# Performance work log

Measured on AMD Instinct MI355X. Metric: run time of the kernel, lower is better.

Reference implementation:

```python
import jax, jax.numpy as jnp
import numpy as np

K_TOP = 8
TEMP = 1.0
GUMBEL_EPS = 1e-20
GEN_EPS = 1e-7
NEG_INF = -1e9


def _genconv(xn, src, dst, e, We, be, W1, b1, W2, b2):
    """GENConv: edge-proj, m=relu(x_src+e)+eps, per-dst softmax aggregation (t=1),
    residual add, then 2-layer MLP."""
    N = xn.shape[0]
    ep = e @ We + be                         # [E, C]
    m = jax.nn.relu(xn[src] + ep) + GEN_EPS  # [E, C]
    mx = jax.ops.segment_max(m, dst, num_segments=N)
    mx = jnp.where(jnp.isfinite(mx), mx, 0.0)
    w = jnp.exp(m - mx[dst])
    den = jax.ops.segment_sum(w, dst, num_segments=N)
    agg = jax.ops.segment_sum(w * m, dst, num_segments=N) / jnp.where(den > 0, den, 1.0)
    out = agg + xn
    return jax.nn.relu(out @ W1 + b1) @ W2 + b2


def setup_inputs() -> dict:
    key = jax.random.key(0)
    ks = jax.random.split(key, 16)
    N, E, D, ED = 1024, 16384, 128, 16
    H1, H2, OUT = 64, 64, 40
    s = 0.02
    return {
        "x": jax.random.normal(ks[0], (N, D), jnp.float32),
        "edge_attr": jax.random.normal(ks[1], (E, ED), jnp.float32),
        "gumbel_u": jax.random.uniform(ks[2], (N, N), jnp.float32),
        "mlp_w": jax.random.normal(ks[3], (ED + 2 * D, 1), jnp.float32) * s,
        "mlp_b": jnp.zeros((1,), jnp.float32),
        "c1_we": jax.random.normal(ks[4], (ED, D), jnp.float32) * s,
        "c1_be": jnp.zeros((D,), jnp.float32),
        "c1_w1": jax.random.normal(ks[5], (D, 2 * D), jnp.float32) * s,
        "c1_b1": jnp.zeros((2 * D,), jnp.float32),
        "c1_w2": jax.random.normal(ks[6], (2 * D, H1), jnp.float32) * s,
        "c1_b2": jnp.zeros((H1,), jnp.float32),
        "c2_we": jax.random.normal(ks[7], (ED, H1), jnp.float32) * s,
        "c2_be": jnp.zeros((H1,), jnp.float32),
        "c2_w1": jax.random.normal(ks[8], (H1, 2 * H1), jnp.float32) * s,
        "c2_b1": jnp.zeros((2 * H1,), jnp.float32),
        "c2_w2": jax.random.normal(ks[9], (2 * H1, H2), jnp.float32) * s,
        "c2_b2": jnp.zeros((H2,), jnp.float32),
        "fc_w": jax.random.normal(ks[10], (H2, OUT), jnp.float32) * s,
        "fc_b": jnp.zeros((OUT,), jnp.float32),
        "num_nodes": N,
        "edge_index": jax.random.randint(ks[11], (2, E), 0, N),
        "node_mask": jnp.ones((N,), jnp.int32),
    }


def reference(x, edge_attr, gumbel_u, mlp_w, mlp_b,
              c1_we, c1_be, c1_w1, c1_b1, c1_w2, c1_b2,
              c2_we, c2_be, c2_w1, c2_b1, c2_w2, c2_b2,
              fc_w, fc_b, num_nodes, edge_index, node_mask):
    N, D = x.shape
    src, dst = edge_index[0], edge_index[1]

    # dense adjacency (duplicate edges sum, only used as a zero/nonzero mask)
    adj = jnp.zeros((N, N), x.dtype).at[src, dst].add(1.0)

    # Edge-score MLP on concat([x_u, x_v*mask, edge_attr_dense]) decomposed
    # linearly (same math as scoring the dense [N,N,2D+ED] feature tensor).
    w_node, w_nb, w_e = mlp_w[:D], mlp_w[D:2 * D], mlp_w[2 * D:]
    s_edge = jnp.zeros((N, N), x.dtype).at[src, dst].set((edge_attr @ w_e)[:, 0])
    score = (x @ w_node) + (x @ w_nb).T * (adj > 0) + s_edge + mlp_b[0]
    score = jnp.where(adj == 0, NEG_INF, score)

    z = jax.nn.softmax(score, axis=-1)
    g = -jnp.log(-jnp.log(gumbel_u + GUMBEL_EPS) + GUMBEL_EPS)
    z = jax.nn.softmax((z + g) / TEMP, axis=-1)

    # top-k edge sampling; softmax output is strictly positive so valid_mask
    # (z>0) is always all-True and shapes stay static at N*k edges.
    _, topi = jax.lax.top_k(z, K_TOP)                       # [N, k]
    new_src = jnp.repeat(jnp.arange(N), K_TOP)
    new_dst = topi.reshape(-1)

    # match each new edge against old edge list (argmax of boolean equality,
    # unmatched edges fall back to index 0 exactly as torch argmax does)
    eq = (edge_index[0][None, :] == new_src[:, None]) & \
         (edge_index[1][None, :] == new_dst[:, None])       # [N*k, E]
    new_attr = edge_attr[jnp.argmax(eq, axis=-1)]

    h = _genconv(x, new_src, new_dst, new_attr, c1_we, c1_be, c1_w1, c1_b1, c1_w2, c1_b2)
    h = jax.nn.relu(h)
    h = _genconv(h, new_src, new_dst, new_attr, c2_we, c2_be, c2_w1, c2_b1, c2_w2, c2_b2)
    h = jax.nn.relu(h)
    out = h @ fc_w + fc_b
    # node_mask is all ones, so x[node_mask != 0] == identity; masked write
    # keeps static shapes under jit.
    return jnp.where((node_mask != 0)[:, None], out, 0.0)
```

## Files before the change

### kernel.cpp

```cpp
#include <hip/hip_runtime.h>
#include <cfloat>

#define NN   1024
#define NE   16384
#define D0   128
#define EDIM 16
#define NH1  64
#define NOUT 40
#define KTOP 8
#define NEGINF (-1000000000.0f)
#define MAXDEG 64
#define PMAX   64

#define OFF_EM  0u
#define OFF_ND  32768u
#define OFF_H   65536u

__device__ __forceinline__ void amx(float& v, int& j, float ov, int oj) {
    if (ov > v || (ov == v && oj < j)) { v = ov; j = oj; }
}

__global__ __launch_bounds__(512) void topk_kernel(
    const float* __restrict__ x, const float* __restrict__ ea,
    const float* __restrict__ u, const float* __restrict__ mlp_w,
    const float* __restrict__ mlp_b, const int* __restrict__ ei,
    const float* __restrict__ c1w1,
    int* __restrict__ nd, int* __restrict__ em)
{
    __shared__ int   idmx[NN];
    __shared__ int   idmn[NN];
    __shared__ float sv[NN];
    __shared__ int   plj[PMAX];
    __shared__ int   ple[PMAX];
    __shared__ int   np;
    __shared__ float wred[16];
    __shared__ float candv[64];
    __shared__ int   candj[64];
    const int i = blockIdx.x, t = threadIdx.x;
    const int lane = t & 63, w = t >> 6;
    const int subl = t & 15;
    const int gg = t >> 4;

    float uval[2];
    uval[0] = u[i * NN + w * 128 + lane];
    uval[1] = u[i * NN + w * 128 + 64 + lane];

    #pragma unroll
    for (int q = 0; q < 2; q++) {
        int j = t + q * 512;
        idmx[j] = -1; idmn[j] = 0x7FFFFFFF; sv[j] = NEGINF;
    }
    if (t == 0) np = 0;
    __syncthreads();

    const int4* s4 = (const int4*)ei;
    #pragma unroll
    for (int q = 0; q < 8; q++) {
        int idx4 = t + q * 512;
        int4 sv4 = s4[idx4];
        int e0 = idx4 * 4;
        if (sv4.x == i) { int dj = ei[NE + e0 + 0]; atomicMax(&idmx[dj], e0 + 0); atomicMin(&idmn[dj], e0 + 0); }
        if (sv4.y == i) { int dj = ei[NE + e0 + 1]; atomicMax(&idmx[dj], e0 + 1); atomicMin(&idmn[dj], e0 + 1); }
        if (sv4.z == i) { int dj = ei[NE + e0 + 2]; atomicMax(&idmx[dj], e0 + 2); atomicMin(&idmn[dj], e0 + 2); }
        if (sv4.w == i) { int dj = ei[NE + e0 + 3]; atomicMax(&idmx[dj], e0 + 3); atomicMin(&idmn[dj], e0 + 3); }
    }
    __syncthreads();

    #pragma unroll
    for (int q = 0; q < 2; q++) {
        int j = t + q * 512;
        int e = idmx[j];
        if (e >= 0) {
            int p = atomicAdd(&np, 1);
            if (p < PMAX) { plj[p] = j; ple[p] = e; }
        }
    }
    __syncthreads();

    float part = x[i * D0 + lane] * mlp_w[lane] + x[i * D0 + 64 + lane] * mlp_w[64 + lane];
    for (int s2 = 32; s2; s2 >>= 1) part += __shfl_down(part, s2);
    const float arb = __shfl(part, 0) + mlp_b[0];

    const int npc = min(np, PMAX);
    for (int p = gg; p < npc; p += 32) {
        int j = plj[p], e = ple[p];
        float pp = ea[e * EDIM + subl] * mlp_w[2 * D0 + subl];
        #pragma unroll
        for (int k = 0; k < 8; k++)
            pp += x[j * D0 + subl + k * 16] * mlp_w[D0 + subl + k * 16];
        #pragma unroll
        for (int s2 = 8; s2; s2 >>= 1) pp += __shfl_down(pp, s2, 16);
        if (subl == 0) sv[j] = pp + arb;
    }
    __syncthreads();

    float val[2];
    val[0] = sv[w * 128 + lane];
    val[1] = sv[w * 128 + 64 + lane];
    float lm = fmaxf(val[0], val[1]);
    for (int s2 = 32; s2; s2 >>= 1) lm = fmaxf(lm, __shfl_down(lm, s2));
    if (lane == 0) wred[w] = lm;
    __syncthreads();
    float rowmax = wred[0];
    #pragma unroll
    for (int q = 1; q < 8; q++) rowmax = fmaxf(rowmax, wred[q]);
    const bool noedge = (rowmax == NEGINF);

    float ls = 0.f;
    #pragma unroll
    for (int q = 0; q < 2; q++) {
        float ev = noedge ? 1.0f : ((val[q] == NEGINF) ? 0.0f : expf(val[q] - rowmax));
        val[q] = ev; ls += ev;
    }
    for (int s2 = 32; s2; s2 >>= 1) ls += __shfl_down(ls, s2);
    if (lane == 0) wred[8 + w] = ls;
    __syncthreads();
    float rsum = wred[8];
    #pragma unroll
    for (int q = 1; q < 8; q++) rsum += wred[8 + q];

    #pragma unroll
    for (int q = 0; q < 2; q++) {
        float g = -logf(-logf(uval[q] + 1e-20f) + 1e-20f);
        val[q] = val[q] / rsum + g;
    }

    for (int sel = 0; sel < KTOP; sel++) {
        float bv = -FLT_MAX; int bj = NN;
        amx(bv, bj, val[0], w * 128 + lane);
        amx(bv, bj, val[1], w * 128 + 64 + lane);
        for (int s2 = 32; s2; s2 >>= 1) {
            float ov = __shfl_down(bv, s2); int oj = __shfl_down(bj, s2);
            amx(bv, bj, ov, oj);
        }
        int wj = __shfl(bj, 0);
        if (lane == 0) { candv[w * KTOP + sel] = bv; candj[w * KTOP + sel] = bj; }
        if (w * 128 + lane == wj) val[0] = -FLT_MAX;
        if (w * 128 + 64 + lane == wj) val[1] = -FLT_MAX;
    }
    __syncthreads();

    if (w == 0) {
        float mv = candv[lane];
        int   mj = candj[lane];
        for (int sel = 0; sel < KTOP; sel++) {
            float bv = mv; int bj = mj;
            for (int s2 = 32; s2; s2 >>= 1) {
                float ov = __shfl_down(bv, s2); int oj = __shfl_down(bj, s2);
                amx(bv, bj, ov, oj);
            }
            int wj = __shfl(bj, 0);
            if (lane == 0) {
                int mn = idmn[wj];
                em[i * KTOP + sel] = (mn == 0x7FFFFFFF) ? 0 : mn;
                nd[i * KTOP + sel] = wj;
            }
            if (mj == wj) mv = -FLT_MAX;
        }
    } else {
        float pf = 0.f;
        if (t < 192)       pf = x[i * D0 + (t - 64)];
        else if (t < 448)  pf = ea[i * 256 + (t - 192)];
        else if (t < 480)  pf = c1w1[i * 32 + (t - 448)];
        asm volatile("" :: "v"(pf));
    }
}

__global__ __launch_bounds__(256) void genconv1_kernel(
    const float* __restrict__ x, const float* __restrict__ ea,
    const float* __restrict__ we_g, const float* __restrict__ be,
    const float* __restrict__ w1, const float* __restrict__ b1,
    const float* __restrict__ w2, const float* __restrict__ b2,
    const int* __restrict__ nd, const int* __restrict__ em,
    float* __restrict__ h)
{
    __shared__ int   slots[MAXDEG];
    __shared__ float eatt[MAXDEG * EDIM];
    __shared__ float arow[D0];
    __shared__ float t1s[2 * D0];
    __shared__ int   cnt_s;
    const int t = threadIdx.x;
    const int r = blockIdx.x;
    if (t == 0) cnt_s = 0;
    __syncthreads();

    const int4* nd4 = (const int4*)nd;
    #pragma unroll
    for (int q = 0; q < 8; q++) {
        int idx4 = t + q * 256;
        int4 v = nd4[idx4];
        int n0 = idx4 * 4;
        if (v.x == r) { int p = atomicAdd(&cnt_s, 1); if (p < MAXDEG) slots[p] = n0 + 0; }
        if (v.y == r) { int p = atomicAdd(&cnt_s, 1); if (p < MAXDEG) slots[p] = n0 + 1; }
        if (v.z == r) { int p = atomicAdd(&cnt_s, 1); if (p < MAXDEG) slots[p] = n0 + 2; }
        if (v.w == r) { int p = atomicAdd(&cnt_s, 1); if (p < MAXDEG) slots[p] = n0 + 3; }
    }
    __syncthreads();
    const int cnt = min(cnt_s, MAXDEG);
    if (t == 0) {
        for (int p = 1; p < cnt; p++) {
            int v = slots[p]; int q = p - 1;
            while (q >= 0 && slots[q] > v) { slots[q + 1] = slots[q]; q--; }
            slots[q + 1] = v;
        }
    }
    __syncthreads();
    for (int q = t; q < cnt * EDIM; q += 256)
        eatt[q] = ea[em[slots[q >> 4]] * EDIM + (q & 15)];
    __syncthreads();

    if (t < D0) {
        const int d = t;
        float wed[EDIM];
        #pragma unroll
        for (int k = 0; k < EDIM; k++) wed[k] = we_g[k * D0 + d];
        const float bed = be[d];

        float mxv = -FLT_MAX;
        for (int idx = 0; idx < cnt; idx++) {
            int src = slots[idx] >> 3;
            float ep = bed;
            #pragma unroll
            for (int k = 0; k < EDIM; k++) ep += eatt[idx * EDIM + k] * wed[k];
            float m = fmaxf(x[src * D0 + d] + ep, 0.f) + 1e-7f;
            mxv = fmaxf(mxv, m);
        }
        float den = 0.f, num = 0.f;
        for (int idx = 0; idx < cnt; idx++) {
            int src = slots[idx] >> 3;
            float ep = bed;
            #pragma unroll
            for (int k = 0; k < EDIM; k++) ep += eatt[idx * EDIM + k] * wed[k];
            float m = fmaxf(x[src * D0 + d] + ep, 0.f) + 1e-7f;
            float w = expf(m - mxv);
            den += w; num += w * m;
        }
        float agg = cnt ? num / (den > 0.f ? den : 1.f) : 0.f;
        arow[d] = agg + x[r * D0 + d];
    }
    __syncthreads();

    {
        float acc = b1[t];
        for (int k = 0; k < D0; k++) acc += arow[k] * w1[k * 2 * D0 + t];
        t1s[t] = fmaxf(acc, 0.f);
    }
    __syncthreads();
    if (t < NH1) {
        float acc = b2[t];
        for (int k = 0; k < 2 * D0; k++) acc += t1s[k] * w2[k * NH1 + t];
        h[r * NH1 + t] = fmaxf(acc, 0.f);
    }
}

__global__ __launch_bounds__(256) void genconv2_kernel(
    const float* __restrict__ h, const float* __restrict__ ea,
    const float* __restrict__ we_g, const float* __restrict__ be,
    const float* __restrict__ w1, const float* __restrict__ b1,
    const float* __restrict__ w2, const float* __restrict__ b2,
    const float* __restrict__ fcw, const float* __restrict__ fcb,
    const int* __restrict__ nd, const int* __restrict__ em,
    const int* __restrict__ mask, float* __restrict__ out)
{
    __shared__ int   slots[MAXDEG];
    __shared__ float eatt[MAXDEG * EDIM];
    __shared__ float arow[NH1];
    __shared__ float t2s[2 * NH1];
    __shared__ float h2s[NH1];
    __shared__ int   cnt_s;
    const int t = threadIdx.x;
    const int r = blockIdx.x;
    if (t == 0) cnt_s = 0;
    __syncthreads();

    const int4* nd4 = (const int4*)nd;
    #pragma unroll
    for (int q = 0; q < 8; q++) {
        int idx4 = t + q * 256;
        int4 v = nd4[idx4];
        int n0 = idx4 * 4;
        if (v.x == r) { int p = atomicAdd(&cnt_s, 1); if (p < MAXDEG) slots[p] = n0 + 0; }
        if (v.y == r) { int p = atomicAdd(&cnt_s, 1); if (p < MAXDEG) slots[p] = n0 + 1; }
        if (v.z == r) { int p = atomicAdd(&cnt_s, 1); if (p < MAXDEG) slots[p] = n0 + 2; }
        if (v.w == r) { int p = atomicAdd(&cnt_s, 1); if (p < MAXDEG) slots[p] = n0 + 3; }
    }
    __syncthreads();
    const int cnt = min(cnt_s, MAXDEG);
    if (t == 0) {
        for (int p = 1; p < cnt; p++) {
            int v = slots[p]; int q = p - 1;
            while (q >= 0 && slots[q] > v) { slots[q + 1] = slots[q]; q--; }
            slots[q + 1] = v;
        }
    }
    __syncthreads();
    for (int q = t; q < cnt * EDIM; q += 256)
        eatt[q] = ea[em[slots[q >> 4]] * EDIM + (q & 15)];
    __syncthreads();

    if (t < NH1) {
        const int d = t;
        float wed[EDIM];
        #pragma unroll
        for (int k = 0; k < EDIM; k++) wed[k] = we_g[k * NH1 + d];
        const float bed = be[d];

        float mxv = -FLT_MAX;
        for (int idx = 0; idx < cnt; idx++) {
            int src = slots[idx] >> 3;
            float ep = bed;
            #pragma unroll
            for (int k = 0; k < EDIM; k++) ep += eatt[idx * EDIM + k] * wed[k];
            float m = fmaxf(h[src * NH1 + d] + ep, 0.f) + 1e-7f;
            mxv = fmaxf(mxv, m);
        }
        float den = 0.f, num = 0.f;
        for (int idx = 0; idx < cnt; idx++) {
            int src = slots[idx] >> 3;
            float ep = bed;
            #pragma unroll
            for (int k = 0; k < EDIM; k++) ep += eatt[idx * EDIM + k] * wed[k];
            float m = fmaxf(h[src * NH1 + d] + ep, 0.f) + 1e-7f;
            float w = expf(m - mxv);
            den += w; num += w * m;
        }
        float agg = cnt ? num / (den > 0.f ? den : 1.f) : 0.f;
        arow[d] = agg + h[r * NH1 + d];
    }
    __syncthreads();

    if (t < 2 * NH1) {
        float acc = b1[t];
        for (int k = 0; k < NH1; k++) acc += arow[k] * w1[k * 2 * NH1 + t];
        t2s[t] = fmaxf(acc, 0.f);
    }
    __syncthreads();
    if (t < NH1) {
        float acc = b2[t];
        for (int k = 0; k < 2 * NH1; k++) acc += t2s[k] * w2[k * NH1 + t];
        h2s[t] = fmaxf(acc, 0.f);
    }
    __syncthreads();
    if (t < NOUT) {
        float acc = fcb[t];
        for (int k = 0; k < NH1; k++) acc += h2s[k] * fcw[k * NOUT + t];
        out[r * NOUT + t] = (mask[r] != 0) ? acc : 0.f;
    }
}

extern "C" void kernel_launch(void* const* d_in, const int* in_sizes, int n_in,
                              void* d_out, int out_size, void* d_ws, size_t ws_size,
                              hipStream_t stream) {
    const float* x      = (const float*)d_in[0];
    const float* ea     = (const float*)d_in[1];
    const float* u      = (const float*)d_in[2];
    const float* mlp_w  = (const float*)d_in[3];
    const float* mlp_b  = (const float*)d_in[4];
    const float* c1_we  = (const float*)d_in[5];
    const float* c1_be  = (const float*)d_in[6];
    const float* c1_w1  = (const float*)d_in[7];
    const float* c1_b1  = (const float*)d_in[8];
    const float* c1_w2  = (const float*)d_in[9];
    const float* c1_b2  = (const float*)d_in[10];
    const float* c2_we  = (const float*)d_in[11];
    const float* c2_be  = (const float*)d_in[12];
    const float* c2_w1  = (const float*)d_in[13];
    const float* c2_b1  = (const float*)d_in[14];
    const float* c2_w2  = (const float*)d_in[15];
    const float* c2_b2  = (const float*)d_in[16];
    const float* fc_w   = (const float*)d_in[17];
    const float* fc_b   = (const float*)d_in[18];
    const int*   ei     = (const int*)d_in[20];
    const int*   mask   = (const int*)d_in[21];

    char* ws = (char*)d_ws;
    int*   em = (int*)(ws + OFF_EM);
    int*   nd = (int*)(ws + OFF_ND);
    float* h  = (float*)(ws + OFF_H);
    float* out = (float*)d_out;

    topk_kernel<<<NN, 512, 0, stream>>>(x, ea, u, mlp_w, mlp_b, ei, c1_w1, nd, em);
    genconv1_kernel<<<NN, 256, 0, stream>>>(x, ea, c1_we, c1_be, c1_w1, c1_b1, c1_w2, c1_b2,
                                            nd, em, h);
    genconv2_kernel<<<NN, 256, 0, stream>>>(h, ea, c2_we, c2_be, c2_w1, c2_b1, c2_w2, c2_b2,
                                            fc_w, fc_b, nd, em, mask, out);
}
```

Before: 156.4 us.

## Precompute per-edge and per-node score terms and bucket edges by source

The edge-scoring MLP is split into three separable dot products: per-edge attribute, per-source and per-destination node terms. A new prep kernel computes these once and buckets edges by source into slot lists with atomics. Each top-k row block then reads only its own edges instead of scanning all 16384 edges. This adds a memset, an extra kernel launch and a fixed per-source capacity of 64 edges, so any edges beyond that would be dropped.

```diff
diff --git a/kernel.cpp b/kernel.cpp
--- a/kernel.cpp
+++ b/kernel.cpp
@@ -10,36 +10,64 @@
 #define KTOP 8
 #define NEGINF (-1000000000.0f)
 #define MAXDEG 64
-#define PMAX   64
-
-#define OFF_EM  0u
-#define OFF_ND  32768u
-#define OFF_H   65536u
+
+#define OFF_CNT   0u
+#define OFF_SE    4096u
+#define OFF_A     69632u
+#define OFF_B     73728u
+#define OFF_SLOT  77824u
+#define OFF_EM    339968u
+#define OFF_ND    372736u
+#define OFF_H     405504u
 
 __device__ __forceinline__ void amx(float& v, int& j, float ov, int oj) {
     if (ov > v || (ov == v && oj < j)) { v = ov; j = oj; }
 }
 
-__global__ __launch_bounds__(512) void topk_kernel(
+__global__ __launch_bounds__(256) void prep_kernel(
     const float* __restrict__ x, const float* __restrict__ ea,
-    const float* __restrict__ u, const float* __restrict__ mlp_w,
+    const float* __restrict__ mlp_w, const int* __restrict__ ei,
+    float* __restrict__ se, float* __restrict__ a, float* __restrict__ b,
+    int* __restrict__ cnt_src, int* __restrict__ slot_src)
+{
+    const int bid = blockIdx.x, t = threadIdx.x;
+    if (bid < 64) {
+        int e = bid * 256 + t;
+        float acc = 0.f;
+        #pragma unroll
+        for (int k = 0; k < EDIM; k++) acc += ea[e * EDIM + k] * mlp_w[2 * D0 + k];
+        se[e] = acc;
+        int s = ei[e];
+        int p = atomicAdd(&cnt_src[s], 1);
+        if (p < MAXDEG) slot_src[s * MAXDEG + p] = e;
+    } else {
+        int lane = t & 63, wid = t >> 6;
+        int row = (bid - 64) * 4 + wid;
+        const float* xr = x + row * D0;
+        float x0 = xr[lane], x1 = xr[64 + lane];
+        float sa = x0 * mlp_w[lane]       + x1 * mlp_w[64 + lane];
+        float sb = x0 * mlp_w[128 + lane] + x1 * mlp_w[192 + lane];
+        for (int s2 = 32; s2; s2 >>= 1) { sa += __shfl_down(sa, s2); sb += __shfl_down(sb, s2); }
+        if (lane == 0) { a[row] = sa; b[row] = sb; }
+    }
+}
+
+__global__ __launch_bounds__(512) void rowtopk_kernel(
+    const float* __restrict__ se, const float* __restrict__ a,
+    const float* __restrict__ b, const float* __restrict__ u,
     const float* __restrict__ mlp_b, const int* __restrict__ ei,
+    const int* __restrict__ cnt_src, const int* __restrict__ slot_src,
+    const float* __restrict__ x, const float* __restrict__ ea,
     const float* __restrict__ c1w1,
     int* __restrict__ nd, int* __restrict__ em)
 {
     __shared__ int   idmx[NN];
     __shared__ int   idmn[NN];
-    __shared__ float sv[NN];
-    __shared__ int   plj[PMAX];
-    __shared__ int   ple[PMAX];
-    __shared__ int   np;
     __shared__ float wred[16];
     __shared__ float candv[64];
     __shared__ int   candj[64];
     const int i = blockIdx.x, t = threadIdx.x;
     const int lane = t & 63, w = t >> 6;
-    const int subl = t & 15;
-    const int gg = t >> 4;
 
     float uval[2];
     uval[0] = u[i * NN + w * 128 + lane];
@@ -48,55 +76,28 @@
     #pragma unroll
     for (int q = 0; q < 2; q++) {
         int j = t + q * 512;
-        idmx[j] = -1; idmn[j] = 0x7FFFFFFF; sv[j] = NEGINF;
-    }
-    if (t == 0) np = 0;
-    __syncthreads();
-
-    const int4* s4 = (const int4*)ei;
-    #pragma unroll
-    for (int q = 0; q < 8; q++) {
-        int idx4 = t + q * 512;
-        int4 sv4 = s4[idx4];
-        int e0 = idx4 * 4;
-        if (sv4.x == i) { int dj = ei[NE + e0 + 0]; atomicMax(&idmx[dj], e0 + 0); atomicMin(&idmn[dj], e0 + 0); }
-        if (sv4.y == i) { int dj = ei[NE + e0 + 1]; atomicMax(&idmx[dj], e0 + 1); atomicMin(&idmn[dj], e0 + 1); }
-        if (sv4.z == i) { int dj = ei[NE + e0 + 2]; atomicMax(&idmx[dj], e0 + 2); atomicMin(&idmn[dj], e0 + 2); }
-        if (sv4.w == i) { int dj = ei[NE + e0 + 3]; atomicMax(&idmx[dj], e0 + 3); atomicMin(&idmn[dj], e0 + 3); }
-    }
-    __syncthreads();
-
+        idmx[j] = -1; idmn[j] = 0x7FFFFFFF;
+    }
+    __syncthreads();
+
+    const int deg = min(cnt_src[i], MAXDEG);
+    if (t < deg) {
+        int e = slot_src[i * MAXDEG + t];
+        int dj = ei[NE + e];
+        atomicMax(&idmx[dj], e);
+        atomicMin(&idmn[dj], e);
+    }
+    __syncthreads();
+
+    const float arb = a[i] + mlp_b[0];
+    float val[2];
     #pragma unroll
     for (int q = 0; q < 2; q++) {
-        int j = t + q * 512;
-        int e = idmx[j];
-        if (e >= 0) {
-            int p = atomicAdd(&np, 1);
-            if (p < PMAX) { plj[p] = j; ple[p] = e; }
-        }
-    }
-    __syncthreads();
-
-    float part = x[i * D0 + lane] * mlp_w[lane] + x[i * D0 + 64 + lane] * mlp_w[64 + lane];
-    for (int s2 = 32; s2; s2 >>= 1) part += __shfl_down(part, s2);
-    const float arb = __shfl(part, 0) + mlp_b[0];
-
-    const int npc = min(np, PMAX);
-    for (int p = gg; p < npc; p += 32) {
-        int j = plj[p], e = ple[p];
-        float pp = ea[e * EDIM + subl] * mlp_w[2 * D0 + subl];
-        #pragma unroll
-        for (int k = 0; k < 8; k++)
-            pp += x[j * D0 + subl + k * 16] * mlp_w[D0 + subl + k * 16];
-        #pragma unroll
-        for (int s2 = 8; s2; s2 >>= 1) pp += __shfl_down(pp, s2, 16);
-        if (subl == 0) sv[j] = pp + arb;
-    }
-    __syncthreads();
-
-    float val[2];
-    val[0] = sv[w * 128 + lane];
-    val[1] = sv[w * 128 + 64 + lane];
+        int j = w * 128 + q * 64 + lane;
+        int id = idmx[j];
+        val[q] = (id >= 0) ? (arb + b[j] + se[id]) : NEGINF;
+    }
+
     float lm = fmaxf(val[0], val[1]);
     for (int s2 = 32; s2; s2 >>= 1) lm = fmaxf(lm, __shfl_down(lm, s2));
     if (lane == 0) wred[w] = lm;
@@ -374,12 +375,20 @@
     const int*   mask   = (const int*)d_in[21];
 
     char* ws = (char*)d_ws;
-    int*   em = (int*)(ws + OFF_EM);
-    int*   nd = (int*)(ws + OFF_ND);
-    float* h  = (float*)(ws + OFF_H);
-    float* out = (float*)d_out;
-
-    topk_kernel<<<NN, 512, 0, stream>>>(x, ea, u, mlp_w, mlp_b, ei, c1_w1, nd, em);
+    int*   cnt_src = (int*)(ws + OFF_CNT);
+    float* se      = (float*)(ws + OFF_SE);
+    float* a       = (float*)(ws + OFF_A);
+    float* b       = (float*)(ws + OFF_B);
+    int*   slot_s  = (int*)(ws + OFF_SLOT);
+    int*   em      = (int*)(ws + OFF_EM);
+    int*   nd      = (int*)(ws + OFF_ND);
+    float* h       = (float*)(ws + OFF_H);
+    float* out     = (float*)d_out;
+
+    hipMemsetAsync(ws + OFF_CNT, 0, 4096, stream);
+    prep_kernel<<<320, 256, 0, stream>>>(x, ea, mlp_w, ei, se, a, b, cnt_src, slot_s);
+    rowtopk_kernel<<<NN, 512, 0, stream>>>(se, a, b, u, mlp_b, ei, cnt_src, slot_s,
+                                           x, ea, c1_w1, nd, em);
     genconv1_kernel<<<NN, 256, 0, stream>>>(x, ea, c1_we, c1_be, c1_w1, c1_b1, c1_w2, c1_b2,
                                             nd, em, h);
     genconv2_kernel<<<NN, 256, 0, stream>>>(h, ea, c2_we, c2_be, c2_w1, c2_b1, c2_w2, c2_b2,
```

Measured after the change: 157.3 us. About the same (+0.6%).
